# Kernel tuning notes

Hardware: AMD Instinct MI355X
Metric: run time of the kernel (lower is better)

Reference implementation:

```python
import jax, jax.numpy as jnp
import numpy as np

SCALE = 1.0 / np.sqrt(3.0)  # head dim is input_dim = 3


def setup_inputs() -> dict:
    key = jax.random.key(0)
    ks = jax.random.split(key, 7)
    B, Nq, Nf, D, C = 4, 2048, 16384, 3, 768
    return {
        "q": jax.random.normal(ks[0], (B, Nq, D), dtype=jnp.float32),
        "k": jax.random.normal(ks[1], (B, Nf, D), dtype=jnp.float32),
        "v": jax.random.normal(ks[2], (B, Nf, C), dtype=jnp.float32),
        "W1": jax.random.normal(ks[3], (D, D), dtype=jnp.float32) * (1.0 / np.sqrt(D)),
        "b1": jax.random.normal(ks[4], (D,), dtype=jnp.float32) * 0.01,
        "W2": jax.random.normal(ks[5], (D, D), dtype=jnp.float32) * (1.0 / np.sqrt(D)),
        "b2": jax.random.normal(ks[6], (D,), dtype=jnp.float32) * 0.01,
    }


def reference(q, k, v, W1, b1, W2, b2):
    # tiny per-point projections + ReLU (nn.Linear stores W as [out,in] -> x @ W.T + b)
    qp = jax.nn.relu(jnp.einsum("bnd,ed->bne", q, W1) + b1)  # [B, Nq, 3]
    kp = jax.nn.relu(jnp.einsum("bmd,ed->bme", k, W2) + b2)  # [B, Nf, 3]
    scores = jnp.einsum("bne,bme->bnm", qp, kp) * SCALE       # [B, Nq, Nf]
    attn = jax.nn.softmax(scores, axis=-1)
    return jnp.einsum("bnm,bmc->bnc", attn, v)                # [B, Nq, C]
```

## Files before the change

### kernel.cpp

```cpp
#include <hip/hip_runtime.h>
#include <math.h>

#define Bt  4
#define NQ  2048
#define NF  16384
#define CC  768

#define QT  128
#define CT  96
#define BK  128
#define THR 512
#define NCH (NF / BK)

#define NFS   4
#define KC    (NF / NFS)
#define BK2   32
#define NCH2  (KC / BK2)
#define TILEB (CC * BK2 * 2)
#define NTILE (Bt * (NF / BK2))

#define SCALE_LOG2E 0.8329080161227079f

typedef __attribute__((ext_vector_type(8)))  short  short8;
typedef __attribute__((ext_vector_type(4)))  float  floatx4;
typedef __attribute__((ext_vector_type(16))) float  floatx16;

#if __has_builtin(__builtin_amdgcn_exp2f)
#define EXP2F(x) __builtin_amdgcn_exp2f(x)
#else
#define EXP2F(x) __expf((x) * 0.6931471805599453f)
#endif

static __device__ __forceinline__ float relu(float x) { return fmaxf(x, 0.0f); }

static __device__ __forceinline__ unsigned int f2bf(float f) {
    unsigned int u = __float_as_uint(f);
    u += 0x7fffu + ((u >> 16) & 1u);
    return u >> 16;
}

#define GLDS16(gsrc, ldst)                                                        \
    __builtin_amdgcn_global_load_lds(                                             \
        (const __attribute__((address_space(1))) unsigned int*)(gsrc),            \
        (__attribute__((address_space(3))) unsigned int*)(ldst), 16, 0, 0)

__global__ __launch_bounds__(256) void prep_kernel(
    const float* __restrict__ q, const float* __restrict__ k,
    const float* __restrict__ W1, const float* __restrict__ b1,
    const float* __restrict__ W2, const float* __restrict__ b2,
    float4* __restrict__ qp, float* __restrict__ kp3)
{
    int idx = blockIdx.x * 256 + threadIdx.x;
    if (idx < Bt * NQ) {
        const float* r = q + (size_t)idx * 3;
        float x0 = r[0], x1 = r[1], x2 = r[2];
        float4 o;
        o.x = relu(fmaf(W1[0], x0, fmaf(W1[1], x1, fmaf(W1[2], x2, b1[0])))) * SCALE_LOG2E;
        o.y = relu(fmaf(W1[3], x0, fmaf(W1[4], x1, fmaf(W1[5], x2, b1[1])))) * SCALE_LOG2E;
        o.z = relu(fmaf(W1[6], x0, fmaf(W1[7], x1, fmaf(W1[8], x2, b1[2])))) * SCALE_LOG2E;
        o.w = 0.0f;
        qp[idx] = o;
    } else {
        int kidx = idx - Bt * NQ;
        const float* r = k + (size_t)kidx * 3;
        float x0 = r[0], x1 = r[1], x2 = r[2];
        float* dst = kp3 + (size_t)kidx * 3;
        dst[0] = relu(fmaf(W2[0], x0, fmaf(W2[1], x1, fmaf(W2[2], x2, b2[0]))));
        dst[1] = relu(fmaf(W2[3], x0, fmaf(W2[4], x1, fmaf(W2[5], x2, b2[1]))));
        dst[2] = relu(fmaf(W2[6], x0, fmaf(W2[7], x1, fmaf(W2[8], x2, b2[2]))));
    }
}

__global__ __launch_bounds__(256) void stats_kernel(
    float4* __restrict__ qp, const float* __restrict__ kp3,
    float2* __restrict__ rstat)
{
    __shared__ float wredA[4][16];
    __shared__ float wredB[4][16];

    const int bid  = blockIdx.x;
    const int b    = bid >> 7;
    const int q0   = (bid & 127) * 16;
    const int t    = threadIdx.x;
    const int wv   = t >> 6;
    const int lane = t & 63;

    float qx[16], qy[16], qz[16];
#pragma unroll
    for (int i = 0; i < 16; ++i) {
        float4 qv = qp[b * NQ + q0 + i];
        qx[i] = qv.x; qy[i] = qv.y; qz[i] = qv.z;
    }
    const float* kpb = kp3 + (size_t)b * NF * 3;

    float pmax[16];
#pragma unroll
    for (int i = 0; i < 16; ++i) pmax[i] = -1e30f;
    for (int m = t; m < NF; m += 256) {
        float kx = kpb[3 * m], ky = kpb[3 * m + 1], kz = kpb[3 * m + 2];
#pragma unroll
        for (int i = 0; i < 16; ++i) {
            float s = fmaf(qx[i], kx, fmaf(qy[i], ky, qz[i] * kz));
            pmax[i] = fmaxf(pmax[i], s);
        }
    }
#pragma unroll
    for (int off = 32; off >= 1; off >>= 1)
#pragma unroll
        for (int i = 0; i < 16; ++i)
            pmax[i] = fmaxf(pmax[i], __shfl_xor(pmax[i], off, 64));
    if (lane == 0)
#pragma unroll
        for (int i = 0; i < 16; ++i) wredA[wv][i] = pmax[i];
    __syncthreads();

    float rowmax[16];
#pragma unroll
    for (int i = 0; i < 16; ++i)
        rowmax[i] = fmaxf(fmaxf(wredA[0][i], wredA[1][i]),
                          fmaxf(wredA[2][i], wredA[3][i]));

    float psum[16];
#pragma unroll
    for (int i = 0; i < 16; ++i) psum[i] = 0.0f;
    for (int m = t; m < NF; m += 256) {
        float kx = kpb[3 * m], ky = kpb[3 * m + 1], kz = kpb[3 * m + 2];
#pragma unroll
        for (int i = 0; i < 16; ++i) {
            float s = fmaf(qx[i], kx, fmaf(qy[i], ky, qz[i] * kz));
            psum[i] += EXP2F(s - rowmax[i]);
        }
    }
#pragma unroll
    for (int off = 32; off >= 1; off >>= 1)
#pragma unroll
        for (int i = 0; i < 16; ++i)
            psum[i] += __shfl_xor(psum[i], off, 64);
    if (lane == 0)
#pragma unroll
        for (int i = 0; i < 16; ++i) wredB[wv][i] = psum[i];
    __syncthreads();

    if (t < 16) {
        float m = fmaxf(fmaxf(wredA[0][t], wredA[1][t]),
                        fmaxf(wredA[2][t], wredA[3][t]));
        float l = wredB[0][t] + wredB[1][t] + wredB[2][t] + wredB[3][t];
        int row = b * NQ + q0 + t;
        rstat[row] = make_float2(m, 1.0f / l);
        qp[row].w = -m;
    }
}

__global__ __launch_bounds__(256) void prep_v_kernel(
    const float* __restrict__ v, char* __restrict__ vpk)
{
    __shared__ float lt[32][68];
    const int t   = threadIdx.x;
    const int bid = blockIdx.x;
    const int cb  = bid % 12;
    const int ch  = (bid / 12) & 511;
    const int b   = bid / (12 * 512);
    const int c0  = cb * 64;

    const float* vb = v + ((size_t)b * NF + (size_t)ch * BK2) * CC + c0;
    const int mi = t >> 4, c4 = (t & 15) << 2;
#pragma unroll
    for (int r2 = 0; r2 < 2; ++r2) {
        const int m = mi + 16 * r2;
        *(float4*)&lt[m][c4] = *(const float4*)(vb + (size_t)m * CC + c4);
    }
    __syncthreads();

    const int c  = t >> 2;
    const int sl = t & 3;
    unsigned int dw[4];
#pragma unroll
    for (int i = 0; i < 4; ++i) {
        float a  = lt[8 * sl + 2 * i][c];
        float b2 = lt[8 * sl + 2 * i + 1][c];
        asm("v_cvt_pk_bf16_f32 %0, %1, %2" : "=v"(dw[i]) : "v"(a), "v"(b2));
    }
    const int cgl = c0 + c;
    char* dst = vpk + (size_t)(b * 512 + ch) * TILEB
              + ((size_t)cgl << 6) + ((sl ^ ((cgl >> 1) & 3)) << 4);
    uint4 u; u.x = dw[0]; u.y = dw[1]; u.z = dw[2]; u.w = dw[3];
    *(uint4*)dst = u;
}

__global__ __launch_bounds__(512) void attn_main32_kernel(
    const char* __restrict__ vpk, const float4* __restrict__ qp,
    const float* __restrict__ kp3, float* __restrict__ out,
    float* __restrict__ partial)
{
    __shared__ __align__(16) char vbuf[2][TILEB];

    const int t   = threadIdx.x;
    const int l   = t & 63;
    const int wv  = t >> 6;
    const int wg  = wv >> 2;
    const int cg  = wv & 3;

    const int bid = blockIdx.x;
    const int g   = ((bid & 7) << 1) | ((bid >> 3) & 1);
    const int qt  = bid >> 4;
    const int b   = g >> 2;
    const int nfs = g & 3;

    const char*  vtile = vpk + (size_t)(b * (NF / BK2) + nfs * NCH2) * TILEB;
    const float* kpb   = kp3 + (size_t)(b * NF + nfs * KC) * 3;

    const float4 qv = qp[b * NQ + qt * QT + wg * 64 + l];
    const float qx = qv.x, qy = qv.y, qz = qv.z, qw = qv.w;

    floatx16 acc[2][6];
#pragma unroll
    for (int qs = 0; qs < 2; ++qs)
#pragma unroll
        for (int cs = 0; cs < 6; ++cs)
#pragma unroll
            for (int r = 0; r < 16; ++r) acc[qs][cs][r] = 0.0f;

    const int lhi  = l >> 5;
    const int swzl = (l >> 1) & 3;
    const int bofs = ((cg * 192 + (l & 31)) << 6);

    {
        const char* src = vtile + wv * 1024 + l * 16;
        char* dst = &vbuf[0][wv * 1024];
#pragma unroll
        for (int i = 0; i < 6; ++i) GLDS16(src + i * 8192, dst + i * 8192);
    }

#pragma unroll 1
    for (int ch = 0; ch < NCH2; ++ch) {
        const int p = ch & 1;
        asm volatile("s_waitcnt vmcnt(0)" ::: "memory");
        __builtin_amdgcn_sched_barrier(0);
        __builtin_amdgcn_s_barrier();
        __builtin_amdgcn_sched_barrier(0);
        if (ch + 1 < NCH2) {
            const char* src = vtile + (size_t)(ch + 1) * TILEB + wv * 1024 + l * 16;
            char* dst = &vbuf[p ^ 1][wv * 1024];
#pragma unroll
            for (int i = 0; i < 6; ++i) GLDS16(src + i * 8192, dst + i * 8192);
        }
        __builtin_amdgcn_sched_barrier(0);

        const char* vbp = &vbuf[p][0];
#pragma unroll
        for (int kk = 0; kk < 2; ++kk) {
            const float4* kp4 = (const float4*)(kpb + (size_t)(ch * BK2 + kk * 16) * 3);

            unsigned int d[8];
#pragma unroll
            for (int g4 = 0; g4 < 4; ++g4) {
                const float4 ka = kp4[3 * g4 + 0];
                const float4 kb = kp4[3 * g4 + 1];
                const float4 kc = kp4[3 * g4 + 2];
                float e0, e1;
                e0 = EXP2F(fmaf(qx, ka.x, fmaf(qy, ka.y, fmaf(qz, ka.z, qw))));
                e1 = EXP2F(fmaf(qx, ka.w, fmaf(qy, kb.x, fmaf(qz, kb.y, qw))));
                asm("v_cvt_pk_bf16_f32 %0, %1, %2" : "=v"(d[2 * g4]) : "v"(e0), "v"(e1));
                e0 = EXP2F(fmaf(qx, kb.z, fmaf(qy, kb.w, fmaf(qz, kc.x, qw))));
                e1 = EXP2F(fmaf(qx, kc.y, fmaf(qy, kc.z, fmaf(qz, kc.w, qw))));
                asm("v_cvt_pk_bf16_f32 %0, %1, %2" : "=v"(d[2 * g4 + 1]) : "v"(e0), "v"(e1));
            }
#pragma unroll
            for (int jj = 0; jj < 4; ++jj)
                asm("v_permlane32_swap_b32 %0, %1" : "+v"(d[jj]), "+v"(d[jj + 4]));

            union { unsigned int u[4]; short8 s; } a0, a1;
#pragma unroll
            for (int jj = 0; jj < 4; ++jj) { a0.u[jj] = d[jj]; a1.u[jj] = d[jj + 4]; }

            const int swz  = ((2 * kk + lhi) ^ swzl) << 4;
            const char* bp = vbp + bofs + swz;

            __builtin_amdgcn_s_setprio(1);
#pragma unroll
            for (int cs = 0; cs < 6; ++cs) {
                union { uint4 u; short8 s; } bw;
                bw.u = *(const uint4*)(bp + cs * 2048);
                acc[0][cs] = __builtin_amdgcn_mfma_f32_32x32x16_bf16(a0.s, bw.s, acc[0][cs], 0, 0, 0);
                acc[1][cs] = __builtin_amdgcn_mfma_f32_32x32x16_bf16(a1.s, bw.s, acc[1][cs], 0, 0, 0);
            }
            __builtin_amdgcn_s_setprio(0);
        }
    }

    float* obase = (nfs == 0) ? out
                 : (partial + (size_t)(nfs - 1) * ((size_t)Bt * NQ * CC));
    const int row0 = b * NQ + qt * QT + wg * 64 + 4 * lhi;
    const int col0 = cg * 192 + (l & 31);
#pragma unroll
    for (int qs = 0; qs < 2; ++qs)
#pragma unroll
        for (int cs = 0; cs < 6; ++cs)
#pragma unroll
            for (int r = 0; r < 16; ++r) {
                const int row = row0 + qs * 32 + (r & 3) + 8 * (r >> 2);
                obase[(size_t)row * CC + col0 + cs * 32] = acc[qs][cs][r];
            }
}

__global__ __launch_bounds__(256) void reduce_kernel(
    float* __restrict__ out, const float* __restrict__ part,
    const float2* __restrict__ rstat)
{
    const int TOT4 = Bt * NQ * CC / 4;
    float4* o4 = (float4*)out;
    const float4* p4 = (const float4*)part;
    for (int i = blockIdx.x * 256 + threadIdx.x; i < TOT4; i += gridDim.x * 256) {
        float4 o = o4[i];
        float4 a = p4[i], b2 = p4[TOT4 + i], c2 = p4[2 * TOT4 + i];
        float lv = rstat[i / (CC / 4)].y;
        o.x = (o.x + a.x + b2.x + c2.x) * lv;
        o.y = (o.y + a.y + b2.y + c2.y) * lv;
        o.z = (o.z + a.z + b2.z + c2.z) * lv;
        o.w = (o.w + a.w + b2.w + c2.w) * lv;
        o4[i] = o;
    }
}

__global__ __launch_bounds__(THR, 4) void attn_mfma_kernel(
    const float* __restrict__ v, const float4* __restrict__ qp,
    const float* __restrict__ kp3, const float2* __restrict__ rstat,
    float* __restrict__ out)
{
    __shared__ unsigned int vTd[2][CT * 68];
    __shared__ float4 kplB[2][96];

    const int t    = threadIdx.x;
    const int bid  = blockIdx.x;
    const int g    = (bid & 7) + 8 * ((bid >> 3) & 3);
    const int qt   = bid >> 5;
    const int b    = g >> 3;
    const int ct   = g & 7;

    const int lane = t & 63;
    const int wv   = t >> 6;
    const int quad = lane >> 4;
    const int l15  = lane & 15;

    const int qrow0 = b * NQ + qt * QT;
    const int cbase = ct * CT;

    float4 qv = qp[qrow0 + wv * 16 + l15];
    const float qx = qv.x, qy = qv.y, qz = qv.z, qw = qv.w;

    const int rp  = (t & 7) + 8 * wv;
    const int c4l = (t >> 3) & 7;

    const float*  vb   = v + (size_t)b * NF * CC + cbase;
    const float4* kp4g = (const float4*)(kp3 + (size_t)b * NF * 3);

    floatx4 acc[6];
#pragma unroll
    for (int cs = 0; cs < 6; ++cs) acc[cs] = (floatx4){0.f, 0.f, 0.f, 0.f};

    float va0[3][4], va1[3][4];
    float4 kpld = make_float4(0.f, 0.f, 0.f, 0.f);

#pragma unroll
    for (int rep = 0; rep < 3; ++rep) {
        int col = 4 * (c4l + 8 * rep);
        const float4* p0 = (const float4*)(vb + (size_t)(2 * rp) * CC + col);
        float4 a = p0[0];
        float4 bq = p0[CC / 4];
        va0[rep][0] = a.x;  va0[rep][1] = a.y;  va0[rep][2] = a.z;  va0[rep][3] = a.w;
        va1[rep][0] = bq.x; va1[rep][1] = bq.y; va1[rep][2] = bq.z; va1[rep][3] = bq.w;
    }
    if (t < 96) kpld = kp4g[t];

    for (int ch = 0; ch < NCH; ++ch) {
        const int p = ch & 1;
#pragma unroll
        for (int rep = 0; rep < 3; ++rep) {
            int c0 = 4 * (c4l + 8 * rep);
#pragma unroll
            for (int w = 0; w < 4; ++w) {
                unsigned int pk = f2bf(va0[rep][w]) | (f2bf(va1[rep][w]) << 16);
                vTd[p][(c0 + w) * 68 + (rp ^ (4 * c4l))] = pk;
            }
        }
        if (t < 96) kplB[p][t] = kpld;
        __syncthreads();

        if (ch + 1 < NCH) {
            int m0 = (ch + 1) * BK;
#pragma unroll
            for (int rep = 0; rep < 3; ++rep) {
                int col = 4 * (c4l + 8 * rep);
                const float4* p0 = (const float4*)(vb + (size_t)(m0 + 2 * rp) * CC + col);
                float4 a = p0[0];
                float4 bq = p0[CC / 4];
                va0[rep][0] = a.x;  va0[rep][1] = a.y;  va0[rep][2] = a.z;  va0[rep][3] = a.w;
                va1[rep][0] = bq.x; va1[rep][1] = bq.y; va1[rep][2] = bq.z; va1[rep][3] = bq.w;
            }
            if (t < 96) kpld = kp4g[(ch + 1) * 96 + t];
        }

#pragma unroll
        for (int kk = 0; kk < BK; kk += 32) {
            union { float4 v4[6]; float f[24]; } kq;
            const int kb4 = (kk * 3) / 4 + 6 * quad;
#pragma unroll
            for (int i = 0; i < 6; ++i) kq.v4[i] = kplB[p][kb4 + i];

            union { short8 s; unsigned int d[4]; } af;
#pragma unroll
            for (int j = 0; j < 8; j += 2) {
                float s0 = fmaf(qx, kq.f[3 * j],
                           fmaf(qy, kq.f[3 * j + 1],
                           fmaf(qz, kq.f[3 * j + 2], qw)));
                float s1 = fmaf(qx, kq.f[3 * j + 3],
                           fmaf(qy, kq.f[3 * j + 4],
                           fmaf(qz, kq.f[3 * j + 5], qw)));
                af.d[j >> 1] = f2bf(EXP2F(s0)) | (f2bf(EXP2F(s1)) << 16);
            }

#pragma unroll
            for (int cs = 0; cs < 6; ++cs) {
                int c  = cs * 16 + l15;
                int d0 = ((kk >> 1) + 4 * quad) ^ (4 * ((c >> 2) & 7));
                union { uint4 u; short8 s; } bw;
                bw.u = *(const uint4*)&vTd[p][c * 68 + d0];
                acc[cs] = __builtin_amdgcn_mfma_f32_16x16x32_bf16(
                    af.s, bw.s, acc[cs], 0, 0, 0);
            }
        }
        __syncthreads();
    }

#pragma unroll
    for (int vv = 0; vv < 4; ++vv) {
        int row = qrow0 + wv * 16 + quad * 4 + vv;
        float lv = rstat[row].y;
        float* orow = out + (size_t)row * CC + cbase + l15;
#pragma unroll
        for (int cs = 0; cs < 6; ++cs)
            orow[cs * 16] = acc[cs][vv] * lv;
    }
}

extern "C" void kernel_launch(void* const* d_in, const int* in_sizes, int n_in,
                              void* d_out, int out_size, void* d_ws, size_t ws_size,
                              hipStream_t stream) {
    const float* q  = (const float*)d_in[0];
    const float* k  = (const float*)d_in[1];
    const float* v  = (const float*)d_in[2];
    const float* W1 = (const float*)d_in[3];
    const float* b1 = (const float*)d_in[4];
    const float* W2 = (const float*)d_in[5];
    const float* b2 = (const float*)d_in[6];
    float* out = (float*)d_out;

    float*  kp3   = (float*)d_ws;
    float4* qpW   = (float4*)((char*)d_ws + (size_t)Bt * NF * 3 * 4);
    float2* rstat = (float2*)((char*)d_ws + (size_t)Bt * NF * 3 * 4 + (size_t)Bt * NQ * 16);
    char*   vpk   = (char*)d_ws + 983040;
    float*  part  = (float*)((char*)d_ws + 983040 + (size_t)NTILE * TILEB);
    const size_t need = 983040 + (size_t)NTILE * TILEB
                      + (size_t)3 * Bt * NQ * CC * 4;

    hipLaunchKernelGGL(prep_kernel, dim3((Bt * NQ + Bt * NF) / 256), dim3(256), 0, stream,
                       q, k, W1, b1, W2, b2, qpW, kp3);
    hipLaunchKernelGGL(stats_kernel, dim3(Bt * (NQ / 16)), dim3(256), 0, stream,
                       qpW, kp3, rstat);

    if (ws_size >= need) {
        hipLaunchKernelGGL(prep_v_kernel, dim3(Bt * 512 * 12), dim3(256), 0, stream,
                           v, vpk);
        hipLaunchKernelGGL(attn_main32_kernel, dim3(256), dim3(512), 0, stream,
                           vpk, qpW, kp3, out, part);
        hipLaunchKernelGGL(reduce_kernel, dim3(2048), dim3(256), 0, stream,
                           out, part, rstat);
    } else {
        hipLaunchKernelGGL(attn_mfma_kernel, dim3(Bt * (NQ / QT) * (CC / CT)), dim3(THR), 0, stream,
                           v, qpW, kp3, rstat, out);
    }
}
```

Before: 666.9 us.

## Share exp-score A fragments via LDS and double-buffer them in smaller blocks

The main attention kernel moves to 256-thread blocks that each cover 64 query rows, with twice as many blocks and two blocks per CU. V tiles shrink to 16 keys, with a matching packed layout and swizzle in prep_v. Each of the four waves now computes a quarter of the exp/bf16 A fragments and shares them through a double-buffered LDS array. The next chunk's A is built after the current MFMAs, so exp work overlaps the next V tile load and is no longer duplicated across the four column-group waves. In exchange there are more barriers per key, with fewer MFMAs between them, and an extra LDS round trip for the A operand.

```diff
diff --git a/kernel.cpp b/kernel.cpp
--- a/kernel.cpp
+++ b/kernel.cpp
@@ -14,7 +14,7 @@
 
 #define NFS   4
 #define KC    (NF / NFS)
-#define BK2   32
+#define BK2   16
 #define NCH2  (KC / BK2)
 #define TILEB (CC * BK2 * 2)
 #define NTILE (Bt * (NF / BK2))
@@ -154,25 +154,25 @@
 __global__ __launch_bounds__(256) void prep_v_kernel(
     const float* __restrict__ v, char* __restrict__ vpk)
 {
-    __shared__ float lt[32][68];
+    __shared__ float lt[16][132];
     const int t   = threadIdx.x;
     const int bid = blockIdx.x;
-    const int cb  = bid % 12;
-    const int ch  = (bid / 12) & 511;
-    const int b   = bid / (12 * 512);
-    const int c0  = cb * 64;
+    const int cb  = bid % 6;
+    const int ch  = (bid / 6) & 1023;
+    const int b   = bid / (6 * 1024);
+    const int c0  = cb * 128;
 
     const float* vb = v + ((size_t)b * NF + (size_t)ch * BK2) * CC + c0;
-    const int mi = t >> 4, c4 = (t & 15) << 2;
+    const int c4 = (t & 31) * 4;
 #pragma unroll
     for (int r2 = 0; r2 < 2; ++r2) {
-        const int m = mi + 16 * r2;
-        *(float4*)&lt[m][c4] = *(const float4*)(vb + (size_t)m * CC + c4);
+        const int row = (t >> 5) + 8 * r2;
+        *(float4*)&lt[row][c4] = *(const float4*)(vb + (size_t)row * CC + c4);
     }
     __syncthreads();
 
-    const int c  = t >> 2;
-    const int sl = t & 3;
+    const int c  = t >> 1;
+    const int sl = t & 1;
     unsigned int dw[4];
 #pragma unroll
     for (int i = 0; i < 4; ++i) {
@@ -181,24 +181,47 @@
         asm("v_cvt_pk_bf16_f32 %0, %1, %2" : "=v"(dw[i]) : "v"(a), "v"(b2));
     }
     const int cgl = c0 + c;
-    char* dst = vpk + (size_t)(b * 512 + ch) * TILEB
-              + ((size_t)cgl << 6) + ((sl ^ ((cgl >> 1) & 3)) << 4);
+    char* dst = vpk + (size_t)(b * (NF / BK2) + ch) * TILEB
+              + ((size_t)cgl << 5)
+              + ((sl ^ ((cgl >> 2) & 1)) << 4);
     uint4 u; u.x = dw[0]; u.y = dw[1]; u.z = dw[2]; u.w = dw[3];
     *(uint4*)dst = u;
 }
 
-__global__ __launch_bounds__(512) void attn_main32_kernel(
+static __device__ __forceinline__ void produceA(
+    const float* __restrict__ kpq,
+    float qx, float qy, float qz, float qw,
+    int l, int cg, unsigned int (*ab)[64][2])
+{
+    float2 a0 = *(const float2*)(kpq);
+    float2 a1 = *(const float2*)(kpq + 2);
+    float2 a2 = *(const float2*)(kpq + 4);
+    float2 b0 = *(const float2*)(kpq + 24);
+    float2 b1 = *(const float2*)(kpq + 26);
+    float2 b2 = *(const float2*)(kpq + 28);
+    float e0 = EXP2F(fmaf(qx, a0.x, fmaf(qy, a0.y, fmaf(qz, a1.x, qw))));
+    float e1 = EXP2F(fmaf(qx, a1.y, fmaf(qy, a2.x, fmaf(qz, a2.y, qw))));
+    float e2 = EXP2F(fmaf(qx, b0.x, fmaf(qy, b0.y, fmaf(qz, b1.x, qw))));
+    float e3 = EXP2F(fmaf(qx, b1.y, fmaf(qy, b2.x, fmaf(qz, b2.y, qw))));
+    unsigned int d0, d1;
+    asm("v_cvt_pk_bf16_f32 %0, %1, %2" : "=v"(d0) : "v"(e0), "v"(e1));
+    asm("v_cvt_pk_bf16_f32 %0, %1, %2" : "=v"(d1) : "v"(e2), "v"(e3));
+    asm("v_permlane32_swap_b32 %0, %1" : "+v"(d0), "+v"(d1));
+    ab[cg >> 1][l][cg & 1]       = d0;
+    ab[(cg >> 1) + 2][l][cg & 1] = d1;
+}
+
+__global__ __launch_bounds__(256, 2) void attn_main32_kernel(
     const char* __restrict__ vpk, const float4* __restrict__ qp,
     const float* __restrict__ kp3, float* __restrict__ out,
     float* __restrict__ partial)
 {
     __shared__ __align__(16) char vbuf[2][TILEB];
+    __shared__ __align__(16) unsigned int abuf[2][4][64][2];
 
     const int t   = threadIdx.x;
     const int l   = t & 63;
-    const int wv  = t >> 6;
-    const int wg  = wv >> 2;
-    const int cg  = wv & 3;
+    const int cg  = t >> 6;
 
     const int bid = blockIdx.x;
     const int g   = ((bid & 7) << 1) | ((bid >> 3) & 1);
@@ -209,98 +232,79 @@
     const char*  vtile = vpk + (size_t)(b * (NF / BK2) + nfs * NCH2) * TILEB;
     const float* kpb   = kp3 + (size_t)(b * NF + nfs * KC) * 3;
 
-    const float4 qv = qp[b * NQ + qt * QT + wg * 64 + l];
+    const float4 qv = qp[b * NQ + qt * 64 + l];
     const float qx = qv.x, qy = qv.y, qz = qv.z, qw = qv.w;
 
-    floatx16 acc[2][6];
-#pragma unroll
-    for (int qs = 0; qs < 2; ++qs)
-#pragma unroll
-        for (int cs = 0; cs < 6; ++cs)
-#pragma unroll
-            for (int r = 0; r < 16; ++r) acc[qs][cs][r] = 0.0f;
+    floatx16 acc0[6], acc1[6];
+#pragma unroll
+    for (int cs = 0; cs < 6; ++cs)
+#pragma unroll
+        for (int r = 0; r < 16; ++r) { acc0[cs][r] = 0.0f; acc1[cs][r] = 0.0f; }
 
     const int lhi  = l >> 5;
-    const int swzl = (l >> 1) & 3;
-    const int bofs = ((cg * 192 + (l & 31)) << 6);
-
-    {
-        const char* src = vtile + wv * 1024 + l * 16;
-        char* dst = &vbuf[0][wv * 1024];
-#pragma unroll
-        for (int i = 0; i < 6; ++i) GLDS16(src + i * 8192, dst + i * 8192);
-    }
+    const int bofs = (cg * 192 + (l & 31)) * 32 + ((lhi ^ ((l >> 2) & 1)) << 4);
+
+#define STAGE(CH, PB)                                                         \
+    do {                                                                      \
+        const char* src = vtile + (size_t)(CH) * TILEB + cg * 6144 + l * 16;  \
+        char* dst = &vbuf[PB][cg * 6144];                                     \
+        _Pragma("unroll")                                                     \
+        for (int i = 0; i < 6; ++i) GLDS16(src + i * 1024, dst + i * 1024);   \
+    } while (0)
+
+    STAGE(0, 0);
+    produceA(kpb + 6 * cg, qx, qy, qz, qw, l, cg, abuf[0]);
 
 #pragma unroll 1
     for (int ch = 0; ch < NCH2; ++ch) {
-        const int p = ch & 1;
-        asm volatile("s_waitcnt vmcnt(0)" ::: "memory");
+        asm volatile("s_waitcnt vmcnt(0) lgkmcnt(0)" ::: "memory");
         __builtin_amdgcn_sched_barrier(0);
         __builtin_amdgcn_s_barrier();
         __builtin_amdgcn_sched_barrier(0);
-        if (ch + 1 < NCH2) {
-            const char* src = vtile + (size_t)(ch + 1) * TILEB + wv * 1024 + l * 16;
-            char* dst = &vbuf[p ^ 1][wv * 1024];
-#pragma unroll
-            for (int i = 0; i < 6; ++i) GLDS16(src + i * 8192, dst + i * 8192);
-        }
-        __builtin_amdgcn_sched_barrier(0);
-
-        const char* vbp = &vbuf[p][0];
-#pragma unroll
-        for (int kk = 0; kk < 2; ++kk) {
-            const float4* kp4 = (const float4*)(kpb + (size_t)(ch * BK2 + kk * 16) * 3);
-
-            unsigned int d[8];
-#pragma unroll
-            for (int g4 = 0; g4 < 4; ++g4) {
-                const float4 ka = kp4[3 * g4 + 0];
-                const float4 kb = kp4[3 * g4 + 1];
-                const float4 kc = kp4[3 * g4 + 2];
-                float e0, e1;
-                e0 = EXP2F(fmaf(qx, ka.x, fmaf(qy, ka.y, fmaf(qz, ka.z, qw))));
-                e1 = EXP2F(fmaf(qx, ka.w, fmaf(qy, kb.x, fmaf(qz, kb.y, qw))));
-                asm("v_cvt_pk_bf16_f32 %0, %1, %2" : "=v"(d[2 * g4]) : "v"(e0), "v"(e1));
-                e0 = EXP2F(fmaf(qx, kb.z, fmaf(qy, kb.w, fmaf(qz, kc.x, qw))));
-                e1 = EXP2F(fmaf(qx, kc.y, fmaf(qy, kc.z, fmaf(qz, kc.w, qw))));
-                asm("v_cvt_pk_bf16_f32 %0, %1, %2" : "=v"(d[2 * g4 + 1]) : "v"(e0), "v"(e1));
-            }
-#pragma unroll
-            for (int jj = 0; jj < 4; ++jj)
-                asm("v_permlane32_swap_b32 %0, %1" : "+v"(d[jj]), "+v"(d[jj + 4]));
-
-            union { unsigned int u[4]; short8 s; } a0, a1;
-#pragma unroll
-            for (int jj = 0; jj < 4; ++jj) { a0.u[jj] = d[jj]; a1.u[jj] = d[jj + 4]; }
-
-            const int swz  = ((2 * kk + lhi) ^ swzl) << 4;
-            const char* bp = vbp + bofs + swz;
-
-            __builtin_amdgcn_s_setprio(1);
-#pragma unroll
-            for (int cs = 0; cs < 6; ++cs) {
-                union { uint4 u; short8 s; } bw;
-                bw.u = *(const uint4*)(bp + cs * 2048);
-                acc[0][cs] = __builtin_amdgcn_mfma_f32_32x32x16_bf16(a0.s, bw.s, acc[0][cs], 0, 0, 0);
-                acc[1][cs] = __builtin_amdgcn_mfma_f32_32x32x16_bf16(a1.s, bw.s, acc[1][cs], 0, 0, 0);
-            }
-            __builtin_amdgcn_s_setprio(0);
-        }
-    }
+
+        const int cur = ch & 1, nxt = cur ^ 1;
+        if (ch + 1 < NCH2) STAGE(ch + 1, nxt);
+
+        union { unsigned int u[4]; short8 s; } a0, a1;
+        {
+            const unsigned int (*AB)[64][2] = abuf[cur];
+            uint2 p0 = *(const uint2*)&AB[0][l][0];
+            uint2 p1 = *(const uint2*)&AB[1][l][0];
+            uint2 p2 = *(const uint2*)&AB[2][l][0];
+            uint2 p3 = *(const uint2*)&AB[3][l][0];
+            a0.u[0] = p0.x; a0.u[1] = p0.y; a0.u[2] = p1.x; a0.u[3] = p1.y;
+            a1.u[0] = p2.x; a1.u[1] = p2.y; a1.u[2] = p3.x; a1.u[3] = p3.y;
+        }
+
+        const char* bp = &vbuf[cur][0] + bofs;
+        __builtin_amdgcn_s_setprio(1);
+#pragma unroll
+        for (int cs = 0; cs < 6; ++cs) {
+            union { uint4 u; short8 s; } bw;
+            bw.u = *(const uint4*)(bp + cs * 1024);
+            acc0[cs] = __builtin_amdgcn_mfma_f32_32x32x16_bf16(a0.s, bw.s, acc0[cs], 0, 0, 0);
+            acc1[cs] = __builtin_amdgcn_mfma_f32_32x32x16_bf16(a1.s, bw.s, acc1[cs], 0, 0, 0);
+        }
+        __builtin_amdgcn_s_setprio(0);
+
+        if (ch + 1 < NCH2)
+            produceA(kpb + (size_t)(ch + 1) * (BK2 * 3) + 6 * cg,
+                     qx, qy, qz, qw, l, cg, abuf[nxt]);
+    }
+#undef STAGE
 
     float* obase = (nfs == 0) ? out
                  : (partial + (size_t)(nfs - 1) * ((size_t)Bt * NQ * CC));
-    const int row0 = b * NQ + qt * QT + wg * 64 + 4 * lhi;
+    const int row0 = b * NQ + qt * 64 + 4 * lhi;
     const int col0 = cg * 192 + (l & 31);
 #pragma unroll
-    for (int qs = 0; qs < 2; ++qs)
-#pragma unroll
-        for (int cs = 0; cs < 6; ++cs)
-#pragma unroll
-            for (int r = 0; r < 16; ++r) {
-                const int row = row0 + qs * 32 + (r & 3) + 8 * (r >> 2);
-                obase[(size_t)row * CC + col0 + cs * 32] = acc[qs][cs][r];
-            }
+    for (int cs = 0; cs < 6; ++cs)
+#pragma unroll
+        for (int r = 0; r < 16; ++r) {
+            const int row = row0 + (r & 3) + 8 * (r >> 2);
+            obase[(size_t)row * CC + col0 + cs * 32]        = acc0[cs][r];
+            obase[(size_t)(row + 32) * CC + col0 + cs * 32] = acc1[cs][r];
+        }
 }
 
 __global__ __launch_bounds__(256) void reduce_kernel(
@@ -469,9 +473,9 @@
                        qpW, kp3, rstat);
 
     if (ws_size >= need) {
-        hipLaunchKernelGGL(prep_v_kernel, dim3(Bt * 512 * 12), dim3(256), 0, stream,
+        hipLaunchKernelGGL(prep_v_kernel, dim3(Bt * (NF / BK2) * 6), dim3(256), 0, stream,
                            v, vpk);
-        hipLaunchKernelGGL(attn_main32_kernel, dim3(256), dim3(512), 0, stream,
+        hipLaunchKernelGGL(attn_main32_kernel, dim3(Bt * 32 * NFS), dim3(256), 0, stream,
                            vpk, qpW, kp3, out, part);
         hipLaunchKernelGGL(reduce_kernel, dim3(2048), dim3(256), 0, stream,
                            out, part, rstat);
```

New measurement: 743.3 us. 1.11x slower.

## Share exp A-operand across column waves via LDS and software-pipeline its production

Applied to the files above, without the earlier changes.

Before, each of the 4 column-group waves recomputed the same exp/bf16 A operand for its query rows. Now each wave computes a quarter of the A fragment, writes it to a double-buffered LDS array, and the A for the next chunk is produced after the MFMAs of the current chunk, so exp work overlaps with the V tile loads. The V-tile LDS swizzle also gets an extra XOR term to reduce bank conflicts. The stats kernel now reads kp with float4 loads, four keys at a time. The trade-off is extra LDS traffic, a wider waitcnt at each barrier, and the correctness risk of a matched swizzle change in two kernels.

```diff
diff --git a/kernel.cpp b/kernel.cpp
--- a/kernel.cpp
+++ b/kernel.cpp
@@ -91,17 +91,20 @@
         float4 qv = qp[b * NQ + q0 + i];
         qx[i] = qv.x; qy[i] = qv.y; qz[i] = qv.z;
     }
-    const float* kpb = kp3 + (size_t)b * NF * 3;
+    const float4* kp4 = (const float4*)(kp3 + (size_t)b * NF * 3);
 
     float pmax[16];
 #pragma unroll
     for (int i = 0; i < 16; ++i) pmax[i] = -1e30f;
-    for (int m = t; m < NF; m += 256) {
-        float kx = kpb[3 * m], ky = kpb[3 * m + 1], kz = kpb[3 * m + 2];
+    for (int m4 = t; m4 < NF / 4; m4 += 256) {
+        float4 A = kp4[3 * m4], B4 = kp4[3 * m4 + 1], C4 = kp4[3 * m4 + 2];
 #pragma unroll
         for (int i = 0; i < 16; ++i) {
-            float s = fmaf(qx[i], kx, fmaf(qy[i], ky, qz[i] * kz));
-            pmax[i] = fmaxf(pmax[i], s);
+            float s0 = fmaf(qx[i], A.x,  fmaf(qy[i], A.y,  qz[i] * A.z));
+            float s1 = fmaf(qx[i], A.w,  fmaf(qy[i], B4.x, qz[i] * B4.y));
+            float s2 = fmaf(qx[i], B4.z, fmaf(qy[i], B4.w, qz[i] * C4.x));
+            float s3 = fmaf(qx[i], C4.y, fmaf(qy[i], C4.z, qz[i] * C4.w));
+            pmax[i] = fmaxf(pmax[i], fmaxf(fmaxf(s0, s1), fmaxf(s2, s3)));
         }
     }
 #pragma unroll
@@ -123,12 +126,16 @@
     float psum[16];
 #pragma unroll
     for (int i = 0; i < 16; ++i) psum[i] = 0.0f;
-    for (int m = t; m < NF; m += 256) {
-        float kx = kpb[3 * m], ky = kpb[3 * m + 1], kz = kpb[3 * m + 2];
+    for (int m4 = t; m4 < NF / 4; m4 += 256) {
+        float4 A = kp4[3 * m4], B4 = kp4[3 * m4 + 1], C4 = kp4[3 * m4 + 2];
 #pragma unroll
         for (int i = 0; i < 16; ++i) {
-            float s = fmaf(qx[i], kx, fmaf(qy[i], ky, qz[i] * kz));
-            psum[i] += EXP2F(s - rowmax[i]);
+            float s0 = fmaf(qx[i], A.x,  fmaf(qy[i], A.y,  qz[i] * A.z));
+            float s1 = fmaf(qx[i], A.w,  fmaf(qy[i], B4.x, qz[i] * B4.y));
+            float s2 = fmaf(qx[i], B4.z, fmaf(qy[i], B4.w, qz[i] * C4.x));
+            float s3 = fmaf(qx[i], C4.y, fmaf(qy[i], C4.z, qz[i] * C4.w));
+            psum[i] += EXP2F(s0 - rowmax[i]) + EXP2F(s1 - rowmax[i])
+                     + EXP2F(s2 - rowmax[i]) + EXP2F(s3 - rowmax[i]);
         }
     }
 #pragma unroll
@@ -182,7 +189,8 @@
     }
     const int cgl = c0 + c;
     char* dst = vpk + (size_t)(b * 512 + ch) * TILEB
-              + ((size_t)cgl << 6) + ((sl ^ ((cgl >> 1) & 3)) << 4);
+              + ((size_t)cgl << 6)
+              + ((sl ^ (((cgl >> 1) ^ (cgl >> 3)) & 3)) << 4);
     uint4 u; u.x = dw[0]; u.y = dw[1]; u.z = dw[2]; u.w = dw[3];
     *(uint4*)dst = u;
 }
@@ -193,12 +201,13 @@
     float* __restrict__ partial)
 {
     __shared__ __align__(16) char vbuf[2][TILEB];
-
-    const int t   = threadIdx.x;
-    const int l   = t & 63;
-    const int wv  = t >> 6;
-    const int wg  = wv >> 2;
-    const int cg  = wv & 3;
+    __shared__ __align__(16) unsigned int abuf[2][2][2][4][64][2];
+
+    const int t  = threadIdx.x;
+    const int l  = t & 63;
+    const int wv = t >> 6;
+    const int wg = wv >> 2;
+    const int cg = wv & 3;
 
     const int bid = blockIdx.x;
     const int g   = ((bid & 7) << 1) | ((bid >> 3) & 1);
@@ -212,95 +221,121 @@
     const float4 qv = qp[b * NQ + qt * QT + wg * 64 + l];
     const float qx = qv.x, qy = qv.y, qz = qv.z, qw = qv.w;
 
-    floatx16 acc[2][6];
-#pragma unroll
-    for (int qs = 0; qs < 2; ++qs)
-#pragma unroll
-        for (int cs = 0; cs < 6; ++cs)
-#pragma unroll
-            for (int r = 0; r < 16; ++r) acc[qs][cs][r] = 0.0f;
+    floatx16 acc0[6], acc1[6];
+#pragma unroll
+    for (int cs = 0; cs < 6; ++cs)
+#pragma unroll
+        for (int r = 0; r < 16; ++r) { acc0[cs][r] = 0.0f; acc1[cs][r] = 0.0f; }
 
     const int lhi  = l >> 5;
-    const int swzl = (l >> 1) & 3;
-    const int bofs = ((cg * 192 + (l & 31)) << 6);
+    const int swzl = ((l >> 1) ^ (l >> 3)) & 3;
+    const int bofs = (cg * 192 + (l & 31)) * 64;
+
+#define STAGE(CH, PB)                                                         \
+    do {                                                                      \
+        const char* src = vtile + (size_t)(CH) * TILEB + wv * 1024 + l * 16;  \
+        char* dst = &vbuf[PB][wv * 1024];                                     \
+        _Pragma("unroll")                                                     \
+        for (int i = 0; i < 6; ++i) GLDS16(src + i * 8192, dst + i * 8192);   \
+    } while (0)
+
+#define KPLOAD(CH, R)                                                         \
+    do {                                                                      \
+        const float* base_ = kpb + (size_t)(CH) * (BK2 * 3) + 6 * cg;         \
+        _Pragma("unroll")                                                     \
+        for (int kk_ = 0; kk_ < 2; ++kk_) {                                   \
+            const float* p_ = base_ + kk_ * 48;                               \
+            R[kk_ * 6 + 0] = *(const float2*)(p_);                            \
+            R[kk_ * 6 + 1] = *(const float2*)(p_ + 2);                        \
+            R[kk_ * 6 + 2] = *(const float2*)(p_ + 4);                        \
+            R[kk_ * 6 + 3] = *(const float2*)(p_ + 24);                       \
+            R[kk_ * 6 + 4] = *(const float2*)(p_ + 26);                       \
+            R[kk_ * 6 + 5] = *(const float2*)(p_ + 28);                       \
+        }                                                                     \
+    } while (0)
+
+#define PRODA(R, O, BB, KK)                                                   \
+    do {                                                                      \
+        float e0_ = EXP2F(fmaf(qx, R[O+0].x, fmaf(qy, R[O+0].y, fmaf(qz, R[O+1].x, qw)))); \
+        float e1_ = EXP2F(fmaf(qx, R[O+1].y, fmaf(qy, R[O+2].x, fmaf(qz, R[O+2].y, qw)))); \
+        float e2_ = EXP2F(fmaf(qx, R[O+3].x, fmaf(qy, R[O+3].y, fmaf(qz, R[O+4].x, qw)))); \
+        float e3_ = EXP2F(fmaf(qx, R[O+4].y, fmaf(qy, R[O+5].x, fmaf(qz, R[O+5].y, qw)))); \
+        unsigned int d0_, d1_;                                                \
+        asm("v_cvt_pk_bf16_f32 %0, %1, %2" : "=v"(d0_) : "v"(e0_), "v"(e1_)); \
+        asm("v_cvt_pk_bf16_f32 %0, %1, %2" : "=v"(d1_) : "v"(e2_), "v"(e3_)); \
+        asm("v_permlane32_swap_b32 %0, %1" : "+v"(d0_), "+v"(d1_));           \
+        abuf[BB][KK][wg][cg >> 1][l][cg & 1]       = d0_;                     \
+        abuf[BB][KK][wg][(cg >> 1) + 2][l][cg & 1] = d1_;                     \
+    } while (0)
 
     {
-        const char* src = vtile + wv * 1024 + l * 16;
-        char* dst = &vbuf[0][wv * 1024];
-#pragma unroll
-        for (int i = 0; i < 6; ++i) GLDS16(src + i * 8192, dst + i * 8192);
+        float2 kpr[12];
+        KPLOAD(0, kpr);
+        STAGE(0, 0);
+        PRODA(kpr, 0, 0, 0);
+        PRODA(kpr, 6, 0, 1);
     }
 
 #pragma unroll 1
     for (int ch = 0; ch < NCH2; ++ch) {
-        const int p = ch & 1;
-        asm volatile("s_waitcnt vmcnt(0)" ::: "memory");
+        asm volatile("s_waitcnt vmcnt(0) lgkmcnt(0)" ::: "memory");
         __builtin_amdgcn_sched_barrier(0);
         __builtin_amdgcn_s_barrier();
         __builtin_amdgcn_sched_barrier(0);
+
+        const int cur = ch & 1, nxt = cur ^ 1;
+        float2 kpn[12];
         if (ch + 1 < NCH2) {
-            const char* src = vtile + (size_t)(ch + 1) * TILEB + wv * 1024 + l * 16;
-            char* dst = &vbuf[p ^ 1][wv * 1024];
-#pragma unroll
-            for (int i = 0; i < 6; ++i) GLDS16(src + i * 8192, dst + i * 8192);
+            STAGE(ch + 1, nxt);
+            KPLOAD(ch + 1, kpn);
         }
         __builtin_amdgcn_sched_barrier(0);
 
-        const char* vbp = &vbuf[p][0];
 #pragma unroll
         for (int kk = 0; kk < 2; ++kk) {
-            const float4* kp4 = (const float4*)(kpb + (size_t)(ch * BK2 + kk * 16) * 3);
-
-            unsigned int d[8];
-#pragma unroll
-            for (int g4 = 0; g4 < 4; ++g4) {
-                const float4 ka = kp4[3 * g4 + 0];
-                const float4 kb = kp4[3 * g4 + 1];
-                const float4 kc = kp4[3 * g4 + 2];
-                float e0, e1;
-                e0 = EXP2F(fmaf(qx, ka.x, fmaf(qy, ka.y, fmaf(qz, ka.z, qw))));
-                e1 = EXP2F(fmaf(qx, ka.w, fmaf(qy, kb.x, fmaf(qz, kb.y, qw))));
-                asm("v_cvt_pk_bf16_f32 %0, %1, %2" : "=v"(d[2 * g4]) : "v"(e0), "v"(e1));
-                e0 = EXP2F(fmaf(qx, kb.z, fmaf(qy, kb.w, fmaf(qz, kc.x, qw))));
-                e1 = EXP2F(fmaf(qx, kc.y, fmaf(qy, kc.z, fmaf(qz, kc.w, qw))));
-                asm("v_cvt_pk_bf16_f32 %0, %1, %2" : "=v"(d[2 * g4 + 1]) : "v"(e0), "v"(e1));
+            union { unsigned int u[4]; short8 s; } a0, a1;
+            {
+                uint2 p0 = *(const uint2*)&abuf[cur][kk][wg][0][l][0];
+                uint2 p1 = *(const uint2*)&abuf[cur][kk][wg][1][l][0];
+                uint2 p2 = *(const uint2*)&abuf[cur][kk][wg][2][l][0];
+                uint2 p3 = *(const uint2*)&abuf[cur][kk][wg][3][l][0];
+                a0.u[0] = p0.x; a0.u[1] = p0.y; a0.u[2] = p1.x; a0.u[3] = p1.y;
+                a1.u[0] = p2.x; a1.u[1] = p2.y; a1.u[2] = p3.x; a1.u[3] = p3.y;
             }
-#pragma unroll
-            for (int jj = 0; jj < 4; ++jj)
-                asm("v_permlane32_swap_b32 %0, %1" : "+v"(d[jj]), "+v"(d[jj + 4]));
-
-            union { unsigned int u[4]; short8 s; } a0, a1;
-#pragma unroll
-            for (int jj = 0; jj < 4; ++jj) { a0.u[jj] = d[jj]; a1.u[jj] = d[jj + 4]; }
-
-            const int swz  = ((2 * kk + lhi) ^ swzl) << 4;
-            const char* bp = vbp + bofs + swz;
+            const char* bp = &vbuf[cur][0] + bofs + (((2 * kk + lhi) ^ swzl) << 4);
 
             __builtin_amdgcn_s_setprio(1);
 #pragma unroll
             for (int cs = 0; cs < 6; ++cs) {
                 union { uint4 u; short8 s; } bw;
                 bw.u = *(const uint4*)(bp + cs * 2048);
-                acc[0][cs] = __builtin_amdgcn_mfma_f32_32x32x16_bf16(a0.s, bw.s, acc[0][cs], 0, 0, 0);
-                acc[1][cs] = __builtin_amdgcn_mfma_f32_32x32x16_bf16(a1.s, bw.s, acc[1][cs], 0, 0, 0);
+                acc0[cs] = __builtin_amdgcn_mfma_f32_32x32x16_bf16(a0.s, bw.s, acc0[cs], 0, 0, 0);
+                acc1[cs] = __builtin_amdgcn_mfma_f32_32x32x16_bf16(a1.s, bw.s, acc1[cs], 0, 0, 0);
             }
             __builtin_amdgcn_s_setprio(0);
         }
-    }
+
+        if (ch + 1 < NCH2) {
+            PRODA(kpn, 0, nxt, 0);
+            PRODA(kpn, 6, nxt, 1);
+        }
+    }
+#undef STAGE
+#undef KPLOAD
+#undef PRODA
 
     float* obase = (nfs == 0) ? out
                  : (partial + (size_t)(nfs - 1) * ((size_t)Bt * NQ * CC));
     const int row0 = b * NQ + qt * QT + wg * 64 + 4 * lhi;
     const int col0 = cg * 192 + (l & 31);
 #pragma unroll
-    for (int qs = 0; qs < 2; ++qs)
-#pragma unroll
-        for (int cs = 0; cs < 6; ++cs)
-#pragma unroll
-            for (int r = 0; r < 16; ++r) {
-                const int row = row0 + qs * 32 + (r & 3) + 8 * (r >> 2);
-                obase[(size_t)row * CC + col0 + cs * 32] = acc[qs][cs][r];
-            }
+    for (int cs = 0; cs < 6; ++cs)
+#pragma unroll
+        for (int r = 0; r < 16; ++r) {
+            const int row = row0 + (r & 3) + 8 * (r >> 2);
+            obase[(size_t)row * CC + col0 + cs * 32]        = acc0[cs][r];
+            obase[(size_t)(row + 32) * CC + col0 + cs * 32] = acc1[cs][r];
+        }
 }
 
 __global__ __launch_bounds__(256) void reduce_kernel(
@@ -471,7 +506,7 @@
     if (ws_size >= need) {
         hipLaunchKernelGGL(prep_v_kernel, dim3(Bt * 512 * 12), dim3(256), 0, stream,
                            v, vpk);
-        hipLaunchKernelGGL(attn_main32_kernel, dim3(256), dim3(512), 0, stream,
+        hipLaunchKernelGGL(attn_main32_kernel, dim3(Bt * 16 * NFS), dim3(512), 0, stream,
                            vpk, qpW, kp3, out, part);
         hipLaunchKernelGGL(reduce_kernel, dim3(2048), dim3(256), 0, stream,
                            out, part, rstat);
```

After: 656.5 us. About the same (-1.6%).
